# Kernel optimization log

Measured on AMD Instinct MI355X. Metric: run time of the kernel, lower is better.

The kernel has to match this reference:

```python
import jax, jax.numpy as jnp
import numpy as np

B, Q_LEN, HIDDEN, N_HEADS, HEAD_DIM = 8, 256, 4096, 32, 128
BLOCK_SIZE, BLOCKS_PER_SEQ, NUM_BLOCKS = 64, 12, 96
MAX_HIST = 512
ROPE_BASE = 10000.0


def setup_inputs() -> dict:
    key = jax.random.key(0)
    ks = jax.random.split(key, 8)
    hidden_states = jax.random.normal(ks[0], (1, B * Q_LEN, HIDDEN), jnp.float32)
    c_attn_w = jax.random.normal(ks[1], (3 * HIDDEN, HIDDEN), jnp.float32) * 0.02
    c_attn_b = jax.random.normal(ks[2], (3 * HIDDEN,), jnp.float32) * 0.02
    c_proj_w = jax.random.normal(ks[3], (HIDDEN, HIDDEN), jnp.float32) * 0.02
    k_cache = jax.random.normal(ks[4], (NUM_BLOCKS, BLOCK_SIZE, N_HEADS, HEAD_DIM), jnp.float32)
    v_cache = jax.random.normal(ks[5], (NUM_BLOCKS, BLOCK_SIZE, N_HEADS, HEAD_DIM), jnp.float32)
    history_lengths = jax.random.randint(ks[6], (B,), 0, MAX_HIST)
    block_offsets = jnp.arange(B * BLOCKS_PER_SEQ, dtype=jnp.int32).reshape(B, BLOCKS_PER_SEQ)
    return dict(hidden_states=hidden_states, c_attn_w=c_attn_w, c_attn_b=c_attn_b,
                c_proj_w=c_proj_w, k_cache=k_cache, v_cache=v_cache,
                history_lengths=history_lengths, block_offsets=block_offsets)


def _rotate_half(x):
    x1, x2 = x[..., :HEAD_DIM // 2], x[..., HEAD_DIM // 2:]
    return jnp.concatenate([-x2, x1], axis=-1)


def reference(hidden_states, c_attn_w, c_attn_b, c_proj_w, k_cache, v_cache,
              history_lengths, block_offsets):
    T = B * Q_LEN  # total tokens (continuous batching, flattened)
    x = hidden_states[0]  # [T, HIDDEN]
    # fused QKV projection
    qkv = x @ c_attn_w.T + c_attn_b  # [T, 3*HIDDEN]
    q, k, v = jnp.split(qkv, 3, axis=-1)
    q = q.reshape(T, N_HEADS, HEAD_DIM)
    k = k.reshape(T, N_HEADS, HEAD_DIM)
    v = v.reshape(T, N_HEADS, HEAD_DIM)
    # per-token absolute positions (position_ids_1d)
    positions = (history_lengths[:, None] + jnp.arange(Q_LEN)).reshape(-1)  # [T]
    # RoPE (ntk_alpha = 1)
    inv_freq = 1.0 / (ROPE_BASE ** (jnp.arange(0, HEAD_DIM, 2, dtype=jnp.float32) / HEAD_DIM))
    freqs = positions.astype(jnp.float32)[:, None] * inv_freq  # [T, D/2]
    emb = jnp.concatenate([freqs, freqs], axis=-1)  # [T, D]
    cos, sin = jnp.cos(emb)[:, None, :], jnp.sin(emb)[:, None, :]

    def rope(t):
        tf = t.astype(jnp.float32)
        return (tf * cos + _rotate_half(tf) * sin).astype(t.dtype)

    q, k = rope(q), rope(k)
    # fill_kv_cache: scatter new K/V into paged blocks at slot = position
    seq_ids = jnp.repeat(jnp.arange(B), Q_LEN)  # [T]
    blk = block_offsets[seq_ids, positions // BLOCK_SIZE]  # [T]
    slot = positions % BLOCK_SIZE  # [T]
    k_cache = k_cache.at[blk, slot].set(k)
    v_cache = v_cache.at[blk, slot].set(v)
    # paged attention: gather each sequence's blocks -> [B, KV, H, D]
    KV = BLOCKS_PER_SEQ * BLOCK_SIZE
    keys = k_cache[block_offsets].reshape(B, KV, N_HEADS, HEAD_DIM)
    vals = v_cache[block_offsets].reshape(B, KV, N_HEADS, HEAD_DIM)
    q_b = q.reshape(B, Q_LEN, N_HEADS, HEAD_DIM)
    scale = 1.0 / jnp.sqrt(jnp.asarray(HEAD_DIM, jnp.float32))
    scores = jnp.einsum('bqhd,bkhd->bhqk', q_b, keys) * scale  # [B,H,Q,KV]
    q_global = history_lengths[:, None] + jnp.arange(Q_LEN)  # [B,Q]
    causal = jnp.arange(KV)[None, None, :] <= q_global[:, :, None]  # [B,Q,KV]
    scores = jnp.where(causal[:, None, :, :], scores, jnp.finfo(scores.dtype).min)
    probs = jax.nn.softmax(scores, axis=-1)
    attn = jnp.einsum('bhqk,bkhd->bqhd', probs, vals).reshape(T, HIDDEN)
    out = attn @ c_proj_w.T  # c_proj (bias-free)
    return out.reshape(1, T, HIDDEN)
```

## Files before the change

kernel.cpp:

```cpp
#include <hip/hip_runtime.h>

typedef unsigned short ushort_t;
typedef float f32x4 __attribute__((ext_vector_type(4)));
typedef _Float16 f16x8 __attribute__((ext_vector_type(8)));
typedef short s16x8 __attribute__((ext_vector_type(8)));

#define NB 8
#define QL 256
#define HID 4096
#define NH 32
#define HD 128

__device__ __forceinline__ _Float16 f2h(float f) { return (_Float16)f; }
__device__ __forceinline__ ushort_t h2u(_Float16 h) {
  union { _Float16 h; ushort_t u; } x; x.h = h; return x.u;
}
__device__ __forceinline__ float u2f(ushort_t u) {
  union { _Float16 h; ushort_t u; } x; x.u = u; return (float)x.h;
}

#define MFMA16H(a, b, c) __builtin_amdgcn_mfma_f32_16x16x32_f16((a), (b), (c), 0, 0, 0)
#define AS1 __attribute__((address_space(1)))
#define AS3 __attribute__((address_space(3)))

__global__ __launch_bounds__(256)
void conv_tile(const float* __restrict__ src, ushort_t* __restrict__ dst,
               int K, int ntiles) {
  const int tile = blockIdx.x * 4 + (threadIdx.x >> 6);
  if (tile >= ntiles) return;
  const int u = threadIdx.x & 63;
  const int row = u >> 2, seg = u & 3;
  const int K32 = K >> 5;
  const int mb = tile / K32, kb = tile % K32;
  const float* sp = src + (size_t)(mb * 16 + row) * K + kb * 32 + seg * 8;
  ushort_t t[8];
#pragma unroll
  for (int j = 0; j < 8; ++j) t[j] = h2u(f2h(sp[j]));
  *(s16x8*)(dst + (size_t)tile * 512 + (((seg << 4) | row) * 8)) = *(s16x8*)t;
}

#define VM4 asm volatile("s_waitcnt vmcnt(4)" ::: "memory")
#define VM0 asm volatile("s_waitcnt vmcnt(0)" ::: "memory")
#define NOSTG

template<int ADD_BIAS, int OUT_F32, int NT>
__global__ __launch_bounds__(256, 3)
void gemm_t(const ushort_t* __restrict__ At, const ushort_t* __restrict__ Bt,
            const float* __restrict__ bias, ushort_t* __restrict__ Ch,
            float* __restrict__ Cf, int N) {
  static_assert(NT % 3 == 2 && NT >= 8, "tail assumes NT%3==2");
  extern __shared__ ushort_t lds[];
  const int nwg = gridDim.x, bid = blockIdx.x;
  const int wg = (bid & 7) * (nwg >> 3) + (bid >> 3);
  const int mi = wg & 15, ni = wg >> 4;
  const int tid = threadIdx.x, w = tid >> 6, l = tid & 63;
  const int l16 = l & 15, lg = l >> 4;
  const int wm = w >> 1, wn = w & 1;

  const ushort_t* sA0 = At + ((size_t)(mi * 8 + 2 * w) * NT) * 512 + l * 8;
  const ushort_t* sA1 = At + ((size_t)(mi * 8 + 2 * w + 1) * NT) * 512 + l * 8;
  const ushort_t* sB0 = Bt + ((size_t)(ni * 8 + 2 * w) * NT) * 512 + l * 8;
  const ushort_t* sB1 = Bt + ((size_t)(ni * 8 + 2 * w + 1) * NT) * 512 + l * 8;

  int aof[4], bof[4];
#pragma unroll
  for (int mf = 0; mf < 4; ++mf) aof[mf] = (wm * 4 + mf) * 512 + l * 8;
#pragma unroll
  for (int nf = 0; nf < 4; ++nf) bof[nf] = 4096 + (wn * 4 + nf) * 512 + l * 8;

  f32x4 acc[4][4];
#pragma unroll
  for (int m = 0; m < 4; ++m)
#pragma unroll
    for (int n = 0; n < 4; ++n) acc[m][n] = (f32x4){0.f, 0.f, 0.f, 0.f};

#define GLDS(srcp, dstofs)                                                    \
  __builtin_amdgcn_global_load_lds((const AS1 void*)(srcp),                   \
                                   (AS3 void*)&lds[dstofs], 16, 0, 0)
#define STG(R, J)                                                             \
  do {                                                                        \
    GLDS(sA0 + (size_t)(J) * 512, (R) * 8192 + (2 * w) * 512);                \
    GLDS(sA1 + (size_t)(J) * 512, (R) * 8192 + (2 * w + 1) * 512);            \
    GLDS(sB0 + (size_t)(J) * 512, (R) * 8192 + 4096 + (2 * w) * 512);         \
    GLDS(sB1 + (size_t)(J) * 512, (R) * 8192 + 4096 + (2 * w + 1) * 512);     \
  } while (0)

#define ITER(R, VMW, STGCODE)                                                 \
  do {                                                                        \
    VMW;                                                                      \
    __builtin_amdgcn_s_barrier();                                             \
    STGCODE;                                                                  \
    f16x8 fa[4], fb[4];                                                       \
    _Pragma("unroll") for (int mf = 0; mf < 4; ++mf)                          \
        fa[mf] = *(const f16x8*)&lds[(R) * 8192 + aof[mf]];                   \
    _Pragma("unroll") for (int nf = 0; nf < 4; ++nf)                          \
        fb[nf] = *(const f16x8*)&lds[(R) * 8192 + bof[nf]];                   \
    asm volatile("s_waitcnt lgkmcnt(0)" ::: "memory");                        \
    __builtin_amdgcn_sched_barrier(0);                                        \
    __builtin_amdgcn_s_setprio(1);                                            \
    _Pragma("unroll") for (int mf = 0; mf < 4; ++mf)                          \
    _Pragma("unroll") for (int nf = 0; nf < 4; ++nf)                          \
        acc[mf][nf] = MFMA16H(fa[mf], fb[nf], acc[mf][nf]);                   \
    __builtin_amdgcn_s_setprio(0);                                            \
  } while (0)

  STG(0, 0);
  STG(1, 1);
  for (int j = 0; j < NT - 2; j += 3) {
    ITER(0, VM4, STG(2, j + 2));
    ITER(1, VM4, STG(0, j + 3));
    ITER(2, VM4, STG(1, j + 4));
  }
  ITER(0, VM4, NOSTG);
  ITER(1, VM0, NOSTG);

#pragma unroll
  for (int nf = 0; nf < 4; ++nf) {
    const int col = ni * 128 + wn * 64 + nf * 16 + l16;
    const float bi = ADD_BIAS ? bias[col] : 0.f;
#pragma unroll
    for (int mf = 0; mf < 4; ++mf) {
      const int row0 = mi * 128 + wm * 64 + mf * 16 + lg * 4;
#pragma unroll
      for (int rr = 0; rr < 4; ++rr) {
        if (OUT_F32)
          Cf[(size_t)(row0 + rr) * N + col] = acc[mf][nf][rr] + bi;
        else
          Ch[(size_t)(row0 + rr) * N + col] = h2u(f2h(acc[mf][nf][rr] + bi));
      }
    }
  }
#undef GLDS
#undef STG
#undef ITER
}

__global__ __launch_bounds__(256)
void rope_inplace(ushort_t* __restrict__ qkv, const int* __restrict__ hist) {
  const int t = blockIdx.x;
  const int b = t >> 8, qq = t & 255;
  __shared__ float cs[64], sn[64];
  const int tid = threadIdx.x;
  if (tid < 64) {
    const float pos = (float)(hist[b] + qq);
    const float f = pos * __expf(-(float)tid * (9.210340371976184f / 64.0f));
    cs[tid] = cosf(f);
    sn[tid] = sinf(f);
  }
  __syncthreads();
  ushort_t* row = qkv + (size_t)t * 12288;
  const int h = tid >> 3;
  const int j0 = (tid & 7) * 8;
  const float qscale = 0.08838834764831845f;
  float c[8], s[8];
#pragma unroll
  for (int j = 0; j < 8; ++j) { c[j] = cs[j0 + j]; s[j] = sn[j0 + j]; }
  {
    ushort_t* p1 = row + h * HD + j0;
    ushort_t* p2 = p1 + 64;
    s16x8 a = *(s16x8*)p1, bb = *(s16x8*)p2;
    ushort_t o1[8], o2[8];
#pragma unroll
    for (int j = 0; j < 8; ++j) {
      const float x1 = u2f((ushort_t)a[j]), x2 = u2f((ushort_t)bb[j]);
      o1[j] = h2u(f2h((x1 * c[j] - x2 * s[j]) * qscale));
      o2[j] = h2u(f2h((x2 * c[j] + x1 * s[j]) * qscale));
    }
    *(s16x8*)p1 = *(s16x8*)o1;
    *(s16x8*)p2 = *(s16x8*)o2;
  }
  {
    ushort_t* p1 = row + HID + h * HD + j0;
    ushort_t* p2 = p1 + 64;
    s16x8 a = *(s16x8*)p1, bb = *(s16x8*)p2;
    ushort_t o1[8], o2[8];
#pragma unroll
    for (int j = 0; j < 8; ++j) {
      const float x1 = u2f((ushort_t)a[j]), x2 = u2f((ushort_t)bb[j]);
      o1[j] = h2u(f2h(x1 * c[j] - x2 * s[j]));
      o2[j] = h2u(f2h(x2 * c[j] + x1 * s[j]));
    }
    *(s16x8*)p1 = *(s16x8*)o1;
    *(s16x8*)p2 = *(s16x8*)o2;
  }
}

__global__ __launch_bounds__(512, 2)
void attn_fwd(const ushort_t* __restrict__ qkv,
              const float* __restrict__ k_cache, const float* __restrict__ v_cache,
              const int* __restrict__ hist, const int* __restrict__ bofs,
              ushort_t* __restrict__ attn_t) {
  const int bh = blockIdx.x;
  const int b = bh >> 5, h = bh & 31;
  const int hb = hist[b];

  __shared__ ushort_t K_lds[64 * 136];
  __shared__ ushort_t V_lds[128 * 72];
  __shared__ ushort_t P_lds[256 * 72];

  const int tid = threadIdx.x;
  const int w = tid >> 6, l = tid & 63;
  const int l16 = l & 15, lg = l >> 4;

  f16x8 qf[2][4];
#pragma unroll
  for (int m = 0; m < 2; ++m) {
    const int qrow = w * 32 + m * 16 + l16;
    const ushort_t* qp = qkv + (size_t)(b * QL + qrow) * 12288 + h * HD + lg * 8;
#pragma unroll
    for (int kd = 0; kd < 4; ++kd) qf[m][kd] = *(const f16x8*)(qp + kd * 32);
  }

  f32x4 o[2][8];
  float mr[2][4], sr[2][4];
#pragma unroll
  for (int m = 0; m < 2; ++m) {
#pragma unroll
    for (int d = 0; d < 8; ++d) o[m][d] = (f32x4){0.f, 0.f, 0.f, 0.f};
#pragma unroll
    for (int r = 0; r < 4; ++r) { mr[m][r] = -1e30f; sr[m][r] = 0.f; }
  }

  const int nt = (hb + QL + 63) >> 6;
  const int srow = tid >> 4;
  const int seg = tid & 15;

  for (int t = 0; t < nt; ++t) {
    const int kv0 = t << 6;
    __syncthreads();
#pragma unroll
    for (int p = 0; p < 2; ++p) {
      const int row = p * 32 + srow;
      const int kvg = kv0 + row;
      if (kvg < hb) {
        const int blk = bofs[b * 12 + t];
        const size_t base = ((size_t)blk * 64 + (kvg & 63)) * HID + h * HD;
        const float* kf = k_cache + base;
        const float* vf = v_cache + base;
        ushort_t tmp[8];
#pragma unroll
        for (int j = 0; j < 8; ++j) tmp[j] = h2u(f2h(kf[seg * 8 + j]));
        *(s16x8*)&K_lds[row * 136 + seg * 8] = *(s16x8*)tmp;
#pragma unroll
        for (int j = 0; j < 8; ++j) {
          const int d = seg + j * 16;
          V_lds[d * 72 + row] = h2u(f2h(vf[d]));
        }
      } else {
        int r2 = kvg - hb;
        if (r2 > QL - 1) r2 = QL - 1;
        const size_t base = (size_t)(b * QL + r2) * 12288 + h * HD;
        const ushort_t* kb = qkv + base + HID;
        const ushort_t* vb = qkv + base + 2 * HID;
        *(s16x8*)&K_lds[row * 136 + seg * 8] = *(const s16x8*)(kb + seg * 8);
#pragma unroll
        for (int j = 0; j < 8; ++j) {
          const int d = seg + j * 16;
          V_lds[d * 72 + row] = vb[d];
        }
      }
    }
    __syncthreads();

    f32x4 sa[2][4];
#pragma unroll
    for (int m = 0; m < 2; ++m)
#pragma unroll
      for (int n = 0; n < 4; ++n) sa[m][n] = (f32x4){0.f, 0.f, 0.f, 0.f};
#pragma unroll
    for (int kd = 0; kd < 4; ++kd) {
      f16x8 kf[4];
#pragma unroll
      for (int n = 0; n < 4; ++n)
        kf[n] = *(const f16x8*)&K_lds[(n * 16 + l16) * 136 + kd * 32 + lg * 8];
#pragma unroll
      for (int m = 0; m < 2; ++m)
#pragma unroll
        for (int n = 0; n < 4; ++n)
          sa[m][n] = MFMA16H(qf[m][kd], kf[n], sa[m][n]);
    }

#pragma unroll
    for (int m = 0; m < 2; ++m) {
#pragma unroll
      for (int n = 0; n < 4; ++n) {
        const int kvg = kv0 + n * 16 + l16;
#pragma unroll
        for (int r = 0; r < 4; ++r) {
          const int qg = hb + w * 32 + m * 16 + lg * 4 + r;
          if (kvg > qg) sa[m][n][r] = -1e30f;
        }
      }
      float tm[4], ts[4];
#pragma unroll
      for (int r = 0; r < 4; ++r)
        tm[r] = fmaxf(fmaxf(sa[m][0][r], sa[m][1][r]),
                      fmaxf(sa[m][2][r], sa[m][3][r]));
#pragma unroll
      for (int x = 1; x < 16; x <<= 1)
#pragma unroll
        for (int r = 0; r < 4; ++r)
          tm[r] = fmaxf(tm[r], __shfl_xor(tm[r], x, 16));
#pragma unroll
      for (int r = 0; r < 4; ++r) {
        const float nm = fmaxf(mr[m][r], tm[r]);
        const float corr = __expf(mr[m][r] - nm);
        mr[m][r] = nm;
        sr[m][r] *= corr;
#pragma unroll
        for (int d = 0; d < 8; ++d) o[m][d][r] *= corr;
        ts[r] = 0.f;
      }
#pragma unroll
      for (int n = 0; n < 4; ++n)
#pragma unroll
        for (int r = 0; r < 4; ++r) {
          const float p = __expf(sa[m][n][r] - mr[m][r]);
          sa[m][n][r] = p;
          ts[r] += p;
        }
#pragma unroll
      for (int x = 1; x < 16; x <<= 1)
#pragma unroll
        for (int r = 0; r < 4; ++r) ts[r] += __shfl_xor(ts[r], x, 16);
#pragma unroll
      for (int r = 0; r < 4; ++r) sr[m][r] += ts[r];
#pragma unroll
      for (int n = 0; n < 4; ++n)
#pragma unroll
        for (int r = 0; r < 4; ++r)
          P_lds[(w * 32 + m * 16 + lg * 4 + r) * 72 + n * 16 + l16] =
              h2u(f2h(sa[m][n][r]));
    }

#pragma unroll
    for (int ks = 0; ks < 2; ++ks) {
      f16x8 pa[2];
#pragma unroll
      for (int m = 0; m < 2; ++m)
        pa[m] = *(const f16x8*)&P_lds[(w * 32 + m * 16 + l16) * 72 + ks * 32 + lg * 8];
#pragma unroll
      for (int d = 0; d < 8; ++d) {
        const f16x8 vb =
            *(const f16x8*)&V_lds[(d * 16 + l16) * 72 + ks * 32 + lg * 8];
#pragma unroll
        for (int m = 0; m < 2; ++m) o[m][d] = MFMA16H(pa[m], vb, o[m][d]);
      }
    }
  }

#pragma unroll
  for (int m = 0; m < 2; ++m) {
    const int rb = b * 16 + w * 2 + m;
#pragma unroll
    for (int r = 0; r < 4; ++r) {
      const float inv = 1.0f / sr[m][r];
#pragma unroll
      for (int d = 0; d < 8; ++d) {
        const int kb = h * 4 + (d >> 1);
        const int lane_dst = (lg * 4 + r) | ((((d & 1) << 1) | (l16 >> 3)) << 4);
        attn_t[((size_t)(rb * 128 + kb)) * 512 + lane_dst * 8 + (l16 & 7)] =
            h2u(f2h(o[m][d][r] * inv));
      }
    }
  }
}

extern "C" void kernel_launch(void* const* d_in, const int* in_sizes, int n_in,
                              void* d_out, int out_size, void* d_ws,
                              size_t ws_size, hipStream_t stream) {
  const float* hidden   = (const float*)d_in[0];
  const float* c_attn_w = (const float*)d_in[1];
  const float* c_attn_b = (const float*)d_in[2];
  const float* c_proj_w = (const float*)d_in[3];
  const float* k_cache  = (const float*)d_in[4];
  const float* v_cache  = (const float*)d_in[5];
  const int* hist       = (const int*)d_in[6];
  const int* bofs       = (const int*)d_in[7];
  float* out = (float*)d_out;

  char* ws = (char*)d_ws;
  const size_t MB = 1ull << 20;
  ushort_t* w_attn_t = (ushort_t*)(ws);
  ushort_t* wproj_t  = (ushort_t*)(ws);
  ushort_t* qkv_h   = (ushort_t*)(ws + 100 * MB);
  ushort_t* attn_t  = (ushort_t*)(ws + 148 * MB);
  ushort_t* x_t     = (ushort_t*)(ws + 196 * MB);

  conv_tile<<<4096, 256, 0, stream>>>(hidden, x_t, 4096, 16384);
  conv_tile<<<24576, 256, 0, stream>>>(c_attn_w, w_attn_t, 4096, 98304);
  gemm_t<1, 0, 128><<<1536, 256, 49152, stream>>>(x_t, w_attn_t, c_attn_b,
                                                  qkv_h, nullptr, 12288);
  rope_inplace<<<2048, 256, 0, stream>>>(qkv_h, hist);
  conv_tile<<<8192, 256, 0, stream>>>(c_proj_w, wproj_t, 4096, 32768);
  attn_fwd<<<256, 512, 0, stream>>>(qkv_h, k_cache, v_cache, hist, bofs,
                                    attn_t);
  gemm_t<0, 1, 128><<<512, 256, 49152, stream>>>(attn_t, wproj_t, nullptr,
                                                 nullptr, out, 4096);
}
```

Before: 427.6 us.

## Enlarge QKV GEMM tile to 256x128 with eight M-fragments per wave

Splits the generic GEMM into a dedicated QKV kernel using a 256x128 output tile (each wave computes 128x64 with 8x4 MFMA fragments), halving the grid to 768 workgroups and raising LDS per stage to 24 KB across three stages. This increases arithmetic intensity per LDS/global load, cutting B-matrix reloads across M tiles. In exchange it doubles accumulator registers and lowers occupancy to 2 workgroups per CU, which may reduce latency hiding; the projection GEMM is unchanged apart from a cleanup.

```diff
diff --git a/kernel.cpp b/kernel.cpp
--- a/kernel.cpp
+++ b/kernel.cpp
@@ -22,6 +22,8 @@
 #define MFMA16H(a, b, c) __builtin_amdgcn_mfma_f32_16x16x32_f16((a), (b), (c), 0, 0, 0)
 #define AS1 __attribute__((address_space(1)))
 #define AS3 __attribute__((address_space(3)))
+#define VMCNT(n) asm volatile("s_waitcnt vmcnt(" #n ")" ::: "memory")
+#define NOSTG
 
 __global__ __launch_bounds__(256)
 void conv_tile(const float* __restrict__ src, ushort_t* __restrict__ dst,
@@ -39,15 +41,103 @@
   *(s16x8*)(dst + (size_t)tile * 512 + (((seg << 4) | row) * 8)) = *(s16x8*)t;
 }
 
-#define VM4 asm volatile("s_waitcnt vmcnt(4)" ::: "memory")
-#define VM0 asm volatile("s_waitcnt vmcnt(0)" ::: "memory")
-#define NOSTG
-
-template<int ADD_BIAS, int OUT_F32, int NT>
+template<int NT>
+__global__ __launch_bounds__(256, 2)
+void gemm_qkv(const ushort_t* __restrict__ At, const ushort_t* __restrict__ Bt,
+              const float* __restrict__ bias, ushort_t* __restrict__ Ch,
+              int N) {
+  static_assert(NT % 3 == 2 && NT >= 8, "tail assumes NT%3==2");
+  extern __shared__ ushort_t lds[];
+  const int nwg = gridDim.x, bid = blockIdx.x;
+  const int wg = (bid & 7) * (nwg >> 3) + (bid >> 3);
+  const int mi = wg & 7, ni = wg >> 3;
+  const int tid = threadIdx.x, w = tid >> 6, l = tid & 63;
+  const int l16 = l & 15, lg = l >> 4;
+  const int wm = w >> 1, wn = w & 1;
+
+  const ushort_t* sA[4];
+  const ushort_t* sB[2];
+#pragma unroll
+  for (int i = 0; i < 4; ++i)
+    sA[i] = At + ((size_t)(mi * 16 + 4 * w + i) * NT) * 512 + l * 8;
+#pragma unroll
+  for (int i = 0; i < 2; ++i)
+    sB[i] = Bt + ((size_t)(ni * 8 + 2 * w + i) * NT) * 512 + l * 8;
+
+  int aof[8], bof[4];
+#pragma unroll
+  for (int mf = 0; mf < 8; ++mf) aof[mf] = (wm * 8 + mf) * 512 + l * 8;
+#pragma unroll
+  for (int nf = 0; nf < 4; ++nf) bof[nf] = 8192 + (wn * 4 + nf) * 512 + l * 8;
+
+  f32x4 acc[8][4];
+#pragma unroll
+  for (int m = 0; m < 8; ++m)
+#pragma unroll
+    for (int n = 0; n < 4; ++n) acc[m][n] = (f32x4){0.f, 0.f, 0.f, 0.f};
+
+#define GLDS(srcp, dstofs)                                                    \
+  __builtin_amdgcn_global_load_lds((const AS1 void*)(srcp),                   \
+                                   (AS3 void*)&lds[dstofs], 16, 0, 0)
+#define STGQ(R, J)                                                            \
+  do {                                                                        \
+    GLDS(sA[0] + (size_t)(J) * 512, (R) * 12288 + (4 * w + 0) * 512);         \
+    GLDS(sA[1] + (size_t)(J) * 512, (R) * 12288 + (4 * w + 1) * 512);         \
+    GLDS(sA[2] + (size_t)(J) * 512, (R) * 12288 + (4 * w + 2) * 512);         \
+    GLDS(sA[3] + (size_t)(J) * 512, (R) * 12288 + (4 * w + 3) * 512);         \
+    GLDS(sB[0] + (size_t)(J) * 512, (R) * 12288 + 8192 + (2 * w + 0) * 512);  \
+    GLDS(sB[1] + (size_t)(J) * 512, (R) * 12288 + 8192 + (2 * w + 1) * 512);  \
+  } while (0)
+
+#define ITERQ(R, VMW, STGCODE)                                                \
+  do {                                                                        \
+    VMW;                                                                      \
+    __builtin_amdgcn_s_barrier();                                             \
+    STGCODE;                                                                  \
+    f16x8 fa[8], fb[4];                                                       \
+    _Pragma("unroll") for (int mf = 0; mf < 8; ++mf)                          \
+        fa[mf] = *(const f16x8*)&lds[(R) * 12288 + aof[mf]];                  \
+    _Pragma("unroll") for (int nf = 0; nf < 4; ++nf)                          \
+        fb[nf] = *(const f16x8*)&lds[(R) * 12288 + bof[nf]];                  \
+    asm volatile("s_waitcnt lgkmcnt(0)" ::: "memory");                        \
+    __builtin_amdgcn_sched_barrier(0);                                        \
+    __builtin_amdgcn_s_setprio(1);                                            \
+    _Pragma("unroll") for (int mf = 0; mf < 8; ++mf)                          \
+    _Pragma("unroll") for (int nf = 0; nf < 4; ++nf)                          \
+        acc[mf][nf] = MFMA16H(fa[mf], fb[nf], acc[mf][nf]);                   \
+    __builtin_amdgcn_s_setprio(0);                                            \
+  } while (0)
+
+  STGQ(0, 0);
+  STGQ(1, 1);
+  for (int j = 0; j < NT - 2; j += 3) {
+    ITERQ(0, VMCNT(6), STGQ(2, j + 2));
+    ITERQ(1, VMCNT(6), STGQ(0, j + 3));
+    ITERQ(2, VMCNT(6), STGQ(1, j + 4));
+  }
+  ITERQ(0, VMCNT(6), NOSTG);
+  ITERQ(1, VMCNT(0), NOSTG);
+
+#pragma unroll
+  for (int nf = 0; nf < 4; ++nf) {
+    const int col = ni * 128 + wn * 64 + nf * 16 + l16;
+    const float bi = bias[col];
+#pragma unroll
+    for (int mf = 0; mf < 8; ++mf) {
+      const int row0 = mi * 256 + wm * 128 + mf * 16 + lg * 4;
+#pragma unroll
+      for (int rr = 0; rr < 4; ++rr)
+        Ch[(size_t)(row0 + rr) * N + col] = h2u(f2h(acc[mf][nf][rr] + bi));
+    }
+  }
+#undef STGQ
+#undef ITERQ
+}
+
+template<int NT>
 __global__ __launch_bounds__(256, 3)
-void gemm_t(const ushort_t* __restrict__ At, const ushort_t* __restrict__ Bt,
-            const float* __restrict__ bias, ushort_t* __restrict__ Ch,
-            float* __restrict__ Cf, int N) {
+void gemm_proj(const ushort_t* __restrict__ At, const ushort_t* __restrict__ Bt,
+               float* __restrict__ Cf, int N) {
   static_assert(NT % 3 == 2 && NT >= 8, "tail assumes NT%3==2");
   extern __shared__ ushort_t lds[];
   const int nwg = gridDim.x, bid = blockIdx.x;
@@ -74,10 +164,7 @@
 #pragma unroll
     for (int n = 0; n < 4; ++n) acc[m][n] = (f32x4){0.f, 0.f, 0.f, 0.f};
 
-#define GLDS(srcp, dstofs)                                                    \
-  __builtin_amdgcn_global_load_lds((const AS1 void*)(srcp),                   \
-                                   (AS3 void*)&lds[dstofs], 16, 0, 0)
-#define STG(R, J)                                                             \
+#define STGP(R, J)                                                            \
   do {                                                                        \
     GLDS(sA0 + (size_t)(J) * 512, (R) * 8192 + (2 * w) * 512);                \
     GLDS(sA1 + (size_t)(J) * 512, (R) * 8192 + (2 * w + 1) * 512);            \
@@ -85,7 +172,7 @@
     GLDS(sB1 + (size_t)(J) * 512, (R) * 8192 + 4096 + (2 * w + 1) * 512);     \
   } while (0)
 
-#define ITER(R, VMW, STGCODE)                                                 \
+#define ITERP(R, VMW, STGCODE)                                                \
   do {                                                                        \
     VMW;                                                                      \
     __builtin_amdgcn_s_barrier();                                             \
@@ -104,35 +191,29 @@
     __builtin_amdgcn_s_setprio(0);                                            \
   } while (0)
 
-  STG(0, 0);
-  STG(1, 1);
+  STGP(0, 0);
+  STGP(1, 1);
   for (int j = 0; j < NT - 2; j += 3) {
-    ITER(0, VM4, STG(2, j + 2));
-    ITER(1, VM4, STG(0, j + 3));
-    ITER(2, VM4, STG(1, j + 4));
-  }
-  ITER(0, VM4, NOSTG);
-  ITER(1, VM0, NOSTG);
+    ITERP(0, VMCNT(4), STGP(2, j + 2));
+    ITERP(1, VMCNT(4), STGP(0, j + 3));
+    ITERP(2, VMCNT(4), STGP(1, j + 4));
+  }
+  ITERP(0, VMCNT(4), NOSTG);
+  ITERP(1, VMCNT(0), NOSTG);
 
 #pragma unroll
   for (int nf = 0; nf < 4; ++nf) {
     const int col = ni * 128 + wn * 64 + nf * 16 + l16;
-    const float bi = ADD_BIAS ? bias[col] : 0.f;
 #pragma unroll
     for (int mf = 0; mf < 4; ++mf) {
       const int row0 = mi * 128 + wm * 64 + mf * 16 + lg * 4;
 #pragma unroll
-      for (int rr = 0; rr < 4; ++rr) {
-        if (OUT_F32)
-          Cf[(size_t)(row0 + rr) * N + col] = acc[mf][nf][rr] + bi;
-        else
-          Ch[(size_t)(row0 + rr) * N + col] = h2u(f2h(acc[mf][nf][rr] + bi));
-      }
-    }
-  }
-#undef GLDS
-#undef STG
-#undef ITER
+      for (int rr = 0; rr < 4; ++rr)
+        Cf[(size_t)(row0 + rr) * N + col] = acc[mf][nf][rr];
+    }
+  }
+#undef STGP
+#undef ITERP
 }
 
 __global__ __launch_bounds__(256)
@@ -389,12 +470,11 @@
 
   conv_tile<<<4096, 256, 0, stream>>>(hidden, x_t, 4096, 16384);
   conv_tile<<<24576, 256, 0, stream>>>(c_attn_w, w_attn_t, 4096, 98304);
-  gemm_t<1, 0, 128><<<1536, 256, 49152, stream>>>(x_t, w_attn_t, c_attn_b,
-                                                  qkv_h, nullptr, 12288);
+  gemm_qkv<128><<<768, 256, 73728, stream>>>(x_t, w_attn_t, c_attn_b, qkv_h,
+                                             12288);
   rope_inplace<<<2048, 256, 0, stream>>>(qkv_h, hist);
   conv_tile<<<8192, 256, 0, stream>>>(c_proj_w, wproj_t, 4096, 32768);
   attn_fwd<<<256, 512, 0, stream>>>(qkv_h, k_cache, v_cache, hist, bofs,
                                     attn_t);
-  gemm_t<0, 1, 128><<<512, 256, 49152, stream>>>(attn_t, wproj_t, nullptr,
-                                                 nullptr, out, 4096);
-}
+  gemm_proj<128><<<512, 256, 49152, stream>>>(attn_t, wproj_t, out, 4096);
+}
```

Measured after the change: 414.2 us. 3.1% less time.
